# Kernel tuning notes

Measured on AMD Instinct MI355X. Metric: run time of the kernel, lower is better.

Reference implementation:

```python
import jax, jax.numpy as jnp
import numpy as np

B, S, D = 2, 2048, 4096
H, HD = 32, 128  # heads, head_dim
ROPE_BASE = 10000.0


def setup_inputs() -> dict:
    key = jax.random.key(0)
    k1, k2, k3 = jax.random.split(key, 3)
    positions = jnp.broadcast_to(jnp.arange(S, dtype=jnp.int64), (B, S))
    hidden_states = jax.random.normal(k1, (B, S, D), dtype=jnp.float32)
    W_qkv = jax.random.normal(k2, (D, 3 * D), dtype=jnp.float32) * (D ** -0.5)
    W_o = jax.random.normal(k3, (D, D), dtype=jnp.float32) * (D ** -0.5)
    return {"positions": positions, "hidden_states": hidden_states, "W_qkv": W_qkv, "W_o": W_o}


def _apply_rope(x, positions):
    # x: [B,S,H,HD]; neox-style rotate-half RoPE
    half = HD // 2
    inv_freq = 1.0 / (ROPE_BASE ** (jnp.arange(0, half, dtype=jnp.float32) / half))
    ang = positions.astype(jnp.float32)[..., None] * inv_freq  # [B,S,half]
    cos = jnp.cos(ang)[:, :, None, :]  # [B,S,1,half]
    sin = jnp.sin(ang)[:, :, None, :]
    x1, x2 = x[..., :half], x[..., half:]
    return jnp.concatenate([x1 * cos - x2 * sin, x2 * cos + x1 * sin], axis=-1)


def reference(positions, hidden_states, W_qkv, W_o):
    qkv = jnp.einsum('bsd,de->bse', hidden_states, W_qkv)
    q, k, v = jnp.split(qkv, 3, axis=-1)
    q = q.reshape(B, S, H, HD)
    k = k.reshape(B, S, H, HD)
    v = v.reshape(B, S, H, HD)
    q = _apply_rope(q, positions)
    k = _apply_rope(k, positions)
    scale = HD ** -0.5
    scores = jnp.einsum('bqhd,bkhd->bhqk', q, k) * scale
    causal = jnp.tril(jnp.ones((S, S), dtype=bool))
    scores = jnp.where(causal[None, None], scores, jnp.finfo(scores.dtype).min)
    probs = jax.nn.softmax(scores, axis=-1)
    attn = jnp.einsum('bhqk,bkhd->bqhd', probs, v).reshape(B, S, D)
    return jnp.einsum('bsd,de->bse', attn, W_o)
```

## Files before the change

kernel.cpp:

```cpp
#include <hip/hip_runtime.h>
#include <hip/hip_bf16.h>
#include <stdint.h>

typedef unsigned short u16;
typedef __attribute__((ext_vector_type(8))) short short8;
typedef __attribute__((ext_vector_type(4))) float f32x4;

__device__ __forceinline__ float bf2f(u16 u) {
  union { uint32_t i; float f; } v; v.i = ((uint32_t)u) << 16; return v.f;
}
__device__ __forceinline__ u16 f2bf(float x) {
  union { float f; uint32_t i; } v; v.f = x;
  uint32_t r = v.i + 0x7FFFu + ((v.i >> 16) & 1u);
  return (u16)(r >> 16);
}
__device__ __forceinline__ void gld16(const void* g, void* l) {
  __builtin_amdgcn_global_load_lds((const __attribute__((address_space(1))) void*)g,
                                   (__attribute__((address_space(3))) void*)l, 16, 0, 0);
}


__global__ __launch_bounds__(256) void cvt_bf16_k(const float* __restrict__ in, u16* __restrict__ out, int n) {
  int i = (blockIdx.x * 256 + threadIdx.x) * 4;
  int stride = gridDim.x * 256 * 4;
  for (; i < n; i += stride) {
    float4 v = *(const float4*)(in + i);
    ushort4 o;
    o.x = f2bf(v.x); o.y = f2bf(v.y); o.z = f2bf(v.z); o.w = f2bf(v.w);
    *(ushort4*)(out + i) = o;
  }
}

__global__ __launch_bounds__(256) void transpose_cvt_k(const float* __restrict__ W, u16* __restrict__ Wt,
                                                        int Kd, int Nd) {
  __shared__ float lds[64][68];
  int t = threadIdx.x;
  int n0 = blockIdx.x * 64, k0 = blockIdx.y * 64;
  int kr = t >> 2, cq = (t & 3) * 16;
  const float* src = W + (size_t)(k0 + kr) * Nd + n0 + cq;
  float4 a = *(const float4*)(src);
  float4 b = *(const float4*)(src + 4);
  float4 c = *(const float4*)(src + 8);
  float4 d = *(const float4*)(src + 12);
  *(float4*)&lds[kr][cq]      = a;
  *(float4*)&lds[kr][cq + 4]  = b;
  *(float4*)&lds[kr][cq + 8]  = c;
  *(float4*)&lds[kr][cq + 12] = d;
  __syncthreads();
  int rn = t >> 2, ks = (t & 3) * 16;
  u16 tmp[16];
  #pragma unroll
  for (int j = 0; j < 16; ++j) tmp[j] = f2bf(lds[ks + j][rn]);
  u16* dst = Wt + (size_t)(n0 + rn) * Kd + k0 + ks;
  *(short8*)dst       = *(short8*)tmp;
  *(short8*)(dst + 8) = *(short8*)(tmp + 8);
}

__global__ __launch_bounds__(64) void rope_table_k(const int* __restrict__ pos, float* __restrict__ tab) {
  int m = blockIdx.x, i = threadIdx.x;
  float p = (float)pos[m];
  float inv = expf(-(float)i * (9.210340371976184f / 64.0f));
  float ang = p * inv;
  float sn, cs;
  sincosf(ang, &sn, &cs);
  tab[m * 128 + i] = cs;
  tab[m * 128 + 64 + i] = sn;
}


__device__ __forceinline__ void stage_half(const u16* __restrict__ G, u16* S, int K,
                                           int tile, int half, int w, int sr, int scsw) {
  int d = tile & 1;
  int sm = half * 8 + w;
  const u16* g = G + (size_t)(sm * 16 + sr) * K + (tile << 6) + scsw;
  u16* s = S + (size_t)(d * 32 + sm * 2) * 512;
  gld16(g, s);
  gld16(g + 32, s + 512);
}

__device__ __forceinline__ short8 frag(const u16* S, int d, int sidx, int kk, int fo) {
  return *(const short8*)&S[(size_t)((d * 32 + sidx * 2 + kk) * 512) + fo];
}

template <int F32OUT>
__global__ __launch_bounds__(512) void gemm256_k(const u16* __restrict__ A, const u16* __restrict__ Bt,
                                                 void* __restrict__ Cp, int N, int K, int GX) {
  __shared__ u16 As[2 * 32 * 512];
  __shared__ u16 Bs[2 * 32 * 512];
  int lid = blockIdx.x;
  int GY = gridDim.x / GX;
  int SY = GY >> 1, SX = GX >> 2;
  int xcd = lid & 7, idx = lid >> 3;
  int ry = xcd >> 2, rx = xcd & 3;
  int bxl = idx / SY, byl = idx - bxl * SY;
  int by = ry * SY + byl, bx = rx * SX + bxl;
  int bm0 = by << 8, bn0 = bx << 8;
  int tid = threadIdx.x, w = tid >> 6, l = tid & 63;
  int wr = w >> 2, wc = w & 3;
  const u16* Ag = A + (size_t)bm0 * K;
  const u16* Bg = Bt + (size_t)bn0 * K;
  int NT = K >> 6;
  int sr = l >> 2;
  int scsw = ((l & 3) * 8) ^ ((sr & 8) ? 16 : 0);
  int fr = l & 15;
  int fo = fr * 32 + (((l >> 4) * 8) ^ ((fr & 8) ? 16 : 0));

  f32x4 acc[8][4];
  #pragma unroll
  for (int i = 0; i < 8; ++i)
    #pragma unroll
    for (int j = 0; j < 4; ++j) acc[i][j] = (f32x4){0.f, 0.f, 0.f, 0.f};

  stage_half(Ag, As, K, 0, 0, w, sr, scsw);
  stage_half(Ag, As, K, 0, 1, w, sr, scsw);
  stage_half(Bg, Bs, K, 0, 0, w, sr, scsw);
  stage_half(Bg, Bs, K, 0, 1, w, sr, scsw);
  stage_half(Ag, As, K, 1, 0, w, sr, scsw);
  asm volatile("s_waitcnt vmcnt(2)" ::: "memory");
  __builtin_amdgcn_s_barrier();
  __builtin_amdgcn_sched_barrier(0);

  for (int t = 0; t < NT; ++t) {
    int d = t & 1;
    short8 a_lo[4][2], a_hi[4][2], b_lo[2][2], b_hi[2][2];
    #pragma unroll
    for (int fm = 0; fm < 4; ++fm) {
      a_lo[fm][0] = frag(As, d, wr * 8 + fm, 0, fo);
      a_lo[fm][1] = frag(As, d, wr * 8 + fm, 1, fo);
    }
    #pragma unroll
    for (int fn = 0; fn < 2; ++fn) {
      b_lo[fn][0] = frag(Bs, d, wc * 4 + fn, 0, fo);
      b_lo[fn][1] = frag(Bs, d, wc * 4 + fn, 1, fo);
    }
    if (t + 1 < NT) stage_half(Ag, As, K, t + 1, 1, w, sr, scsw);
    __builtin_amdgcn_s_barrier();
    __builtin_amdgcn_s_setprio(1);
    #pragma unroll
    for (int fn = 0; fn < 2; ++fn) {
      b_hi[fn][0] = frag(Bs, d, wc * 4 + 2 + fn, 0, fo);
      b_hi[fn][1] = frag(Bs, d, wc * 4 + 2 + fn, 1, fo);
    }
    #pragma unroll
    for (int fm = 0; fm < 4; ++fm)
      #pragma unroll
      for (int fn = 0; fn < 2; ++fn) {
        acc[fm][fn] = __builtin_amdgcn_mfma_f32_16x16x32_bf16(a_lo[fm][0], b_lo[fn][0], acc[fm][fn], 0, 0, 0);
        acc[fm][fn] = __builtin_amdgcn_mfma_f32_16x16x32_bf16(a_lo[fm][1], b_lo[fn][1], acc[fm][fn], 0, 0, 0);
      }
    __builtin_amdgcn_s_setprio(0);
    __builtin_amdgcn_s_barrier();
    if (t + 1 < NT) stage_half(Bg, Bs, K, t + 1, 0, w, sr, scsw);
    __builtin_amdgcn_s_barrier();
    __builtin_amdgcn_s_setprio(1);
    #pragma unroll
    for (int fm = 0; fm < 4; ++fm) {
      a_hi[fm][0] = frag(As, d, wr * 8 + 4 + fm, 0, fo);
      a_hi[fm][1] = frag(As, d, wr * 8 + 4 + fm, 1, fo);
    }
    #pragma unroll
    for (int fm = 0; fm < 4; ++fm)
      #pragma unroll
      for (int fn = 0; fn < 2; ++fn) {
        acc[fm][2 + fn] = __builtin_amdgcn_mfma_f32_16x16x32_bf16(a_lo[fm][0], b_hi[fn][0], acc[fm][2 + fn], 0, 0, 0);
        acc[fm][2 + fn] = __builtin_amdgcn_mfma_f32_16x16x32_bf16(a_lo[fm][1], b_hi[fn][1], acc[fm][2 + fn], 0, 0, 0);
      }
    __builtin_amdgcn_s_setprio(0);
    __builtin_amdgcn_s_barrier();
    if (t + 1 < NT) stage_half(Bg, Bs, K, t + 1, 1, w, sr, scsw);
    __builtin_amdgcn_s_barrier();
    __builtin_amdgcn_s_setprio(1);
    #pragma unroll
    for (int fm = 0; fm < 4; ++fm)
      #pragma unroll
      for (int fn = 0; fn < 2; ++fn) {
        acc[4 + fm][2 + fn] = __builtin_amdgcn_mfma_f32_16x16x32_bf16(a_hi[fm][0], b_hi[fn][0], acc[4 + fm][2 + fn], 0, 0, 0);
        acc[4 + fm][2 + fn] = __builtin_amdgcn_mfma_f32_16x16x32_bf16(a_hi[fm][1], b_hi[fn][1], acc[4 + fm][2 + fn], 0, 0, 0);
      }
    __builtin_amdgcn_s_setprio(0);
    __builtin_amdgcn_s_barrier();
    if (t + 2 < NT) stage_half(Ag, As, K, t + 2, 0, w, sr, scsw);
    __builtin_amdgcn_s_setprio(1);
    #pragma unroll
    for (int fm = 0; fm < 4; ++fm)
      #pragma unroll
      for (int fn = 0; fn < 2; ++fn) {
        acc[4 + fm][fn] = __builtin_amdgcn_mfma_f32_16x16x32_bf16(a_hi[fm][0], b_lo[fn][0], acc[4 + fm][fn], 0, 0, 0);
        acc[4 + fm][fn] = __builtin_amdgcn_mfma_f32_16x16x32_bf16(a_hi[fm][1], b_lo[fn][1], acc[4 + fm][fn], 0, 0, 0);
      }
    __builtin_amdgcn_s_setprio(0);
    if (t + 2 < NT) asm volatile("s_waitcnt vmcnt(2)" ::: "memory");
    else            asm volatile("s_waitcnt vmcnt(0)" ::: "memory");
    __builtin_amdgcn_s_barrier();
    __builtin_amdgcn_sched_barrier(0);
  }

  int r0 = bm0 + wr * 128 + ((l >> 4) << 2);
  int c0 = bn0 + wc * 64 + (l & 15);
  #pragma unroll
  for (int fm = 0; fm < 8; ++fm)
    #pragma unroll
    for (int fn = 0; fn < 4; ++fn)
      #pragma unroll
      for (int r = 0; r < 4; ++r) {
        size_t idx2 = (size_t)(r0 + fm * 16 + r) * N + (c0 + fn * 16);
        if (F32OUT) ((float*)Cp)[idx2] = acc[fm][fn][r];
        else        ((u16*)Cp)[idx2]   = f2bf(acc[fm][fn][r]);
      }
}


__global__ __launch_bounds__(256) void rope_qk_k(const u16* __restrict__ qkv, const float* __restrict__ tab,
                                                  u16* __restrict__ Qb, u16* __restrict__ Kb) {
  int m = blockIdx.x, t = threadIdx.x;
  int b = m >> 11, s = m & 2047;
  const float* tabm = tab + m * 128;
  #pragma unroll
  for (int part = 0; part < 2; ++part) {
    const u16* src = qkv + (size_t)m * 12288 + part * 4096;
    u16* dst = part ? Kb : Qb;
    float qs = part ? 1.0f : 0.08838834764831845f;
    #pragma unroll
    for (int it = 0; it < 2; ++it) {
      int v = t + it * 256;
      int h = v >> 4;
      int d1 = (v & 15) * 4;
      const u16* sp = src + h * 128 + d1;
      ushort4 x1 = *(const ushort4*)(sp);
      ushort4 x2 = *(const ushort4*)(sp + 64);
      float4 cs = *(const float4*)(tabm + d1);
      float4 sn = *(const float4*)(tabm + 64 + d1);
      ushort4 o1, o2;
      o1.x = f2bf((bf2f(x1.x) * cs.x - bf2f(x2.x) * sn.x) * qs);
      o1.y = f2bf((bf2f(x1.y) * cs.y - bf2f(x2.y) * sn.y) * qs);
      o1.z = f2bf((bf2f(x1.z) * cs.z - bf2f(x2.z) * sn.z) * qs);
      o1.w = f2bf((bf2f(x1.w) * cs.w - bf2f(x2.w) * sn.w) * qs);
      o2.x = f2bf((bf2f(x2.x) * cs.x + bf2f(x1.x) * sn.x) * qs);
      o2.y = f2bf((bf2f(x2.y) * cs.y + bf2f(x1.y) * sn.y) * qs);
      o2.z = f2bf((bf2f(x2.z) * cs.z + bf2f(x1.z) * sn.z) * qs);
      o2.w = f2bf((bf2f(x2.w) * cs.w + bf2f(x1.w) * sn.w) * qs);
      u16* o = dst + ((size_t)(b * 32 + h) * 2048 + s) * 128 + d1;
      *(ushort4*)o        = o1;
      *(ushort4*)(o + 64) = o2;
    }
  }
}

__global__ __launch_bounds__(256) void v_transpose_k(const u16* __restrict__ qkv, u16* __restrict__ Vt) {
  __shared__ u16 lds[64][136];
  int bid = blockIdx.x;
  int bh = bid >> 5, st = bid & 31;
  int b = bh >> 5, h = bh & 31;
  int s0 = st * 64;
  int t = threadIdx.x;
  int r = t >> 2, cq = (t & 3) * 32;
  const u16* src = qkv + (size_t)(b * 2048 + s0 + r) * 12288 + 8192 + h * 128 + cq;
  *(short8*)&lds[r][cq]      = *(const short8*)(src);
  *(short8*)&lds[r][cq + 8]  = *(const short8*)(src + 8);
  *(short8*)&lds[r][cq + 16] = *(const short8*)(src + 16);
  *(short8*)&lds[r][cq + 24] = *(const short8*)(src + 24);
  __syncthreads();
  int d = t >> 1, sseg = (t & 1) * 32;
  u16 tmp[32];
  #pragma unroll
  for (int j = 0; j < 32; ++j) tmp[j] = lds[sseg + j][d];
  u16* o = Vt + (size_t)bh * (128 * 2048) + (size_t)d * 2048 + s0 + sseg;
  *(short8*)(o)      = *(short8*)(tmp);
  *(short8*)(o + 8)  = *(short8*)(tmp + 8);
  *(short8*)(o + 16) = *(short8*)(tmp + 16);
  *(short8*)(o + 24) = *(short8*)(tmp + 24);
}


__device__ __forceinline__ void stage_kv(const u16* __restrict__ Kg, const u16* __restrict__ Vg,
                                         u16* Ksb, u16* Vsb, int j0, int w, int l) {
  #pragma unroll
  for (int c = 0; c < 2; ++c) {
    int rk = c * 32 + w * 4 + (l >> 4);
    int kcol = ((l & 15) * 8) ^ ((rk & 7) << 3);
    gld16(Kg + (size_t)(j0 + rk) * 128 + kcol, Ksb + (c * 32 + w * 4) * 128);
    int rv = c * 64 + w * 8 + (l >> 3);
    int vcol = ((l & 7) * 8) ^ ((rv & 7) << 3);
    gld16(Vg + (size_t)rv * 2048 + j0 + vcol, Vsb + (c * 64 + w * 8) * 64);
  }
}

__global__ __launch_bounds__(512, 2) void attn_k(const u16* __restrict__ Qb, const u16* __restrict__ Kb,
                                                  const u16* __restrict__ Vt, u16* __restrict__ attnb) {
  __shared__ u16 Ks[2][64 * 128];
  __shared__ u16 Vs[2][128 * 64];
  __shared__ u16 Ps[8][32 * 64];
  int lid = blockIdx.x + gridDim.x * blockIdx.y;
  int xcd = lid & 7, idx = lid >> 3;
  int bh = xcd * 8 + (idx >> 3);
  int qt = idx & 7;
  int b = bh >> 5, h = bh & 31;
  int q0 = qt * 256;
  int t = threadIdx.x, w = t >> 6, l = t & 63;
  int g = l >> 4, fr = l & 15;
  const u16* Qg = Qb + (size_t)bh * (2048 * 128);
  const u16* Kg = Kb + (size_t)bh * (2048 * 128);
  const u16* Vg = Vt + (size_t)bh * (128 * 2048);

  short8 aq[2][4];
  #pragma unroll
  for (int fm = 0; fm < 2; ++fm)
    #pragma unroll
    for (int kk = 0; kk < 4; ++kk)
      aq[fm][kk] = *(const short8*)&Qg[(size_t)(q0 + w * 32 + fm * 16 + fr) * 128 + kk * 32 + g * 8];

  stage_kv(Kg, Vg, Ks[0], Vs[0], 0, w, l);
  __syncthreads();

  f32x4 zero = {0.f, 0.f, 0.f, 0.f};
  f32x4 o[2][8];
  #pragma unroll
  for (int fm = 0; fm < 2; ++fm)
    #pragma unroll
    for (int fd = 0; fd < 8; ++fd) o[fm][fd] = zero;
  float m_run[2][4], l_run[2][4];
  #pragma unroll
  for (int fm = 0; fm < 2; ++fm)
    #pragma unroll
    for (int r = 0; r < 4; ++r) { m_run[fm][r] = -1e30f; l_run[fm][r] = 0.f; }

  int NJ = 4 * qt + 4;
  for (int j = 0; j < NJ; ++j) {
    int j0 = j * 64;
    int cur = j & 1;
    if (j + 1 < NJ) stage_kv(Kg, Vg, Ks[cur ^ 1], Vs[cur ^ 1], j0 + 64, w, l);
    if (j0 < q0 + w * 32 + 32) {
      f32x4 sc[2][4];
      #pragma unroll
      for (int fm = 0; fm < 2; ++fm)
        #pragma unroll
        for (int fn = 0; fn < 4; ++fn) sc[fm][fn] = zero;
      __builtin_amdgcn_s_setprio(1);
      #pragma unroll
      for (int kk = 0; kk < 4; ++kk) {
        #pragma unroll
        for (int fn = 0; fn < 4; ++fn) {
          short8 bk = *(const short8*)&Ks[cur][(fn * 16 + fr) * 128 + ((kk * 32 + g * 8) ^ ((fr & 7) << 3))];
          #pragma unroll
          for (int fm = 0; fm < 2; ++fm)
            sc[fm][fn] = __builtin_amdgcn_mfma_f32_16x16x32_bf16(aq[fm][kk], bk, sc[fm][fn], 0, 0, 0);
        }
      }
      __builtin_amdgcn_s_setprio(0);
      int qb_ = q0 + w * 32 + (g << 2);
      int kb_ = j0 + fr;
      #pragma unroll
      for (int fm = 0; fm < 2; ++fm)
        #pragma unroll
        for (int fn = 0; fn < 4; ++fn)
          #pragma unroll
          for (int r = 0; r < 4; ++r)
            if (kb_ + fn * 16 > qb_ + fm * 16 + r) sc[fm][fn][r] = -1e30f;
      float mx[2][4];
      #pragma unroll
      for (int fm = 0; fm < 2; ++fm)
        #pragma unroll
        for (int r = 0; r < 4; ++r) {
          float v = fmaxf(fmaxf(sc[fm][0][r], sc[fm][1][r]), fmaxf(sc[fm][2][r], sc[fm][3][r]));
          v = fmaxf(v, __shfl_xor(v, 1));
          v = fmaxf(v, __shfl_xor(v, 2));
          v = fmaxf(v, __shfl_xor(v, 4));
          v = fmaxf(v, __shfl_xor(v, 8));
          mx[fm][r] = v;
        }
      float scale[2][4];
      #pragma unroll
      for (int fm = 0; fm < 2; ++fm)
        #pragma unroll
        for (int r = 0; r < 4; ++r) {
          float mn = fmaxf(m_run[fm][r], mx[fm][r]);
          scale[fm][r] = __expf(m_run[fm][r] - mn);
          m_run[fm][r] = mn;
        }
      float rs[2][4];
      #pragma unroll
      for (int fm = 0; fm < 2; ++fm)
        #pragma unroll
        for (int r = 0; r < 4; ++r) {
          float acc = 0.f;
          #pragma unroll
          for (int fn = 0; fn < 4; ++fn) {
            float p = __expf(sc[fm][fn][r] - m_run[fm][r]);
            sc[fm][fn][r] = p;
            acc += p;
          }
          acc += __shfl_xor(acc, 1);
          acc += __shfl_xor(acc, 2);
          acc += __shfl_xor(acc, 4);
          acc += __shfl_xor(acc, 8);
          rs[fm][r] = acc;
        }
      #pragma unroll
      for (int fm = 0; fm < 2; ++fm)
        #pragma unroll
        for (int r = 0; r < 4; ++r) l_run[fm][r] = l_run[fm][r] * scale[fm][r] + rs[fm][r];
      #pragma unroll
      for (int fm = 0; fm < 2; ++fm)
        #pragma unroll
        for (int fd = 0; fd < 8; ++fd)
          #pragma unroll
          for (int r = 0; r < 4; ++r) o[fm][fd][r] *= scale[fm][r];
      #pragma unroll
      for (int fm = 0; fm < 2; ++fm)
        #pragma unroll
        for (int fn = 0; fn < 4; ++fn)
          #pragma unroll
          for (int r = 0; r < 4; ++r) {
            int prow = fm * 16 + (g << 2) + r;
            Ps[w][prow * 64 + ((fn * 16 + fr) ^ ((prow & 7) << 3))] = f2bf(sc[fm][fn][r]);
          }
      __builtin_amdgcn_s_setprio(1);
      #pragma unroll
      for (int kk = 0; kk < 2; ++kk) {
        short8 pa[2];
        #pragma unroll
        for (int fm = 0; fm < 2; ++fm)
          pa[fm] = *(const short8*)&Ps[w][(fm * 16 + fr) * 64 + ((kk * 32 + g * 8) ^ ((fr & 7) << 3))];
        #pragma unroll
        for (int fd = 0; fd < 8; ++fd) {
          short8 bv = *(const short8*)&Vs[cur][(fd * 16 + fr) * 64 + ((kk * 32 + g * 8) ^ ((fr & 7) << 3))];
          #pragma unroll
          for (int fm = 0; fm < 2; ++fm)
            o[fm][fd] = __builtin_amdgcn_mfma_f32_16x16x32_bf16(pa[fm], bv, o[fm][fd], 0, 0, 0);
        }
      }
      __builtin_amdgcn_s_setprio(0);
    }
    __syncthreads();
  }

  #pragma unroll
  for (int fm = 0; fm < 2; ++fm)
    #pragma unroll
    for (int r = 0; r < 4; ++r) {
      float inv = 1.0f / l_run[fm][r];
      int srow = q0 + w * 32 + fm * 16 + (g << 2) + r;
      u16* dst = attnb + (size_t)(b * 2048 + srow) * 4096 + h * 128 + fr;
      #pragma unroll
      for (int fd = 0; fd < 8; ++fd)
        dst[fd * 16] = f2bf(o[fm][fd][r] * inv);
    }
}


extern "C" void kernel_launch(void* const* d_in, const int* in_sizes, int n_in,
                              void* d_out, int out_size, void* d_ws, size_t ws_size,
                              hipStream_t stream) {
  const int*   positions = (const int*)d_in[0];
  const float* hidden    = (const float*)d_in[1];
  const float* W_qkv     = (const float*)d_in[2];
  const float* W_o       = (const float*)d_in[3];
  float* out = (float*)d_out;
  char* ws = (char*)d_ws;

  u16* R0 = (u16*)ws;
  u16* R1 = (u16*)(ws + 100663296);
  u16* R2 = (u16*)(ws + 201326592);
  float* tab = (float*)(ws + 234881024);

  u16* hidden_bf = R2;
  u16* Wqkv_t = R0;
  u16* qkv = R1;
  u16* Qb = R2;
  u16* Kb = R0;
  u16* Vt = R0 + 16777216;
  u16* attnb = R0 + 33554432;
  u16* Wo_t = R1;

  cvt_bf16_k<<<4096, 256, 0, stream>>>(hidden, hidden_bf, 16777216);
  transpose_cvt_k<<<dim3(192, 64), 256, 0, stream>>>(W_qkv, Wqkv_t, 4096, 12288);
  rope_table_k<<<4096, 64, 0, stream>>>(positions, tab);

  gemm256_k<0><<<768, 512, 0, stream>>>(hidden_bf, Wqkv_t, qkv, 12288, 4096, 48);

  rope_qk_k<<<4096, 256, 0, stream>>>(qkv, tab, Qb, Kb);
  v_transpose_k<<<2048, 256, 0, stream>>>(qkv, Vt);
  transpose_cvt_k<<<dim3(64, 64), 256, 0, stream>>>(W_o, Wo_t, 4096, 4096);

  attn_k<<<dim3(8, 64), 512, 0, stream>>>(Qb, Kb, Vt, attnb);

  gemm256_k<1><<<256, 512, 0, stream>>>(attnb, Wo_t, out, 4096, 4096, 16);
}
```

Baseline: 894.9 us.

## Fuse RoPE, Q scaling and V transpose into QKV GEMM epilogue

```diff
diff --git a/kernel.cpp b/kernel.cpp
--- a/kernel.cpp
+++ b/kernel.cpp
@@ -57,14 +57,15 @@
 }
 
 __global__ __launch_bounds__(64) void rope_table_k(const int* __restrict__ pos, float* __restrict__ tab) {
-  int m = blockIdx.x, i = threadIdx.x;
+  int m = blockIdx.x * 64 + threadIdx.x;
   float p = (float)pos[m];
-  float inv = expf(-(float)i * (9.210340371976184f / 64.0f));
-  float ang = p * inv;
-  float sn, cs;
-  sincosf(ang, &sn, &cs);
-  tab[m * 128 + i] = cs;
-  tab[m * 128 + 64 + i] = sn;
+  for (int i = 0; i < 64; ++i) {
+    float inv = expf(-(float)i * (9.210340371976184f / 64.0f));
+    float sn, cs;
+    sincosf(p * inv, &sn, &cs);
+    tab[i * 4096 + m] = cs;
+    tab[(64 + i) * 4096 + m] = sn;
+  }
 }
 
 
@@ -82,9 +83,12 @@
   return *(const short8*)&S[(size_t)((d * 32 + sidx * 2 + kk) * 512) + fo];
 }
 
-template <int F32OUT>
+template <int MODE>
 __global__ __launch_bounds__(512) void gemm256_k(const u16* __restrict__ A, const u16* __restrict__ Bt,
-                                                 void* __restrict__ Cp, int N, int K, int GX) {
+                                                 void* __restrict__ Cp, int N, int K, int GX,
+                                                 const float* __restrict__ tab,
+                                                 u16* __restrict__ Qb, u16* __restrict__ Kb,
+                                                 u16* __restrict__ Vt) {
   __shared__ u16 As[2 * 32 * 512];
   __shared__ u16 Bs[2 * 32 * 512];
   int lid = blockIdx.x;
@@ -103,7 +107,8 @@
   int sr = l >> 2;
   int scsw = ((l & 3) * 8) ^ ((sr & 8) ? 16 : 0);
   int fr = l & 15;
-  int fo = fr * 32 + (((l >> 4) * 8) ^ ((fr & 8) ? 16 : 0));
+  int g = l >> 4;
+  int fo = fr * 32 + ((g * 8) ^ ((fr & 8) ? 16 : 0));
 
   f32x4 acc[8][4];
   #pragma unroll
@@ -137,36 +142,36 @@
     __builtin_amdgcn_s_barrier();
     __builtin_amdgcn_s_setprio(1);
     #pragma unroll
+    for (int fm = 0; fm < 4; ++fm)
+      #pragma unroll
+      for (int fn = 0; fn < 2; ++fn) {
+        acc[fm][fn] = __builtin_amdgcn_mfma_f32_16x16x32_bf16(a_lo[fm][0], b_lo[fn][0], acc[fm][fn], 0, 0, 0);
+        acc[fm][fn] = __builtin_amdgcn_mfma_f32_16x16x32_bf16(a_lo[fm][1], b_lo[fn][1], acc[fm][fn], 0, 0, 0);
+      }
+    __builtin_amdgcn_s_setprio(0);
+    __builtin_amdgcn_s_barrier();
+    #pragma unroll
     for (int fn = 0; fn < 2; ++fn) {
       b_hi[fn][0] = frag(Bs, d, wc * 4 + 2 + fn, 0, fo);
       b_hi[fn][1] = frag(Bs, d, wc * 4 + 2 + fn, 1, fo);
     }
+    if (t + 1 < NT) stage_half(Bg, Bs, K, t + 1, 0, w, sr, scsw);
+    __builtin_amdgcn_s_barrier();
+    __builtin_amdgcn_s_setprio(1);
     #pragma unroll
     for (int fm = 0; fm < 4; ++fm)
       #pragma unroll
       for (int fn = 0; fn < 2; ++fn) {
-        acc[fm][fn] = __builtin_amdgcn_mfma_f32_16x16x32_bf16(a_lo[fm][0], b_lo[fn][0], acc[fm][fn], 0, 0, 0);
-        acc[fm][fn] = __builtin_amdgcn_mfma_f32_16x16x32_bf16(a_lo[fm][1], b_lo[fn][1], acc[fm][fn], 0, 0, 0);
+        acc[fm][2 + fn] = __builtin_amdgcn_mfma_f32_16x16x32_bf16(a_lo[fm][0], b_hi[fn][0], acc[fm][2 + fn], 0, 0, 0);
+        acc[fm][2 + fn] = __builtin_amdgcn_mfma_f32_16x16x32_bf16(a_lo[fm][1], b_hi[fn][1], acc[fm][2 + fn], 0, 0, 0);
       }
     __builtin_amdgcn_s_setprio(0);
     __builtin_amdgcn_s_barrier();
-    if (t + 1 < NT) stage_half(Bg, Bs, K, t + 1, 0, w, sr, scsw);
-    __builtin_amdgcn_s_barrier();
-    __builtin_amdgcn_s_setprio(1);
     #pragma unroll
     for (int fm = 0; fm < 4; ++fm) {
       a_hi[fm][0] = frag(As, d, wr * 8 + 4 + fm, 0, fo);
       a_hi[fm][1] = frag(As, d, wr * 8 + 4 + fm, 1, fo);
     }
-    #pragma unroll
-    for (int fm = 0; fm < 4; ++fm)
-      #pragma unroll
-      for (int fn = 0; fn < 2; ++fn) {
-        acc[fm][2 + fn] = __builtin_amdgcn_mfma_f32_16x16x32_bf16(a_lo[fm][0], b_hi[fn][0], acc[fm][2 + fn], 0, 0, 0);
-        acc[fm][2 + fn] = __builtin_amdgcn_mfma_f32_16x16x32_bf16(a_lo[fm][1], b_hi[fn][1], acc[fm][2 + fn], 0, 0, 0);
-      }
-    __builtin_amdgcn_s_setprio(0);
-    __builtin_amdgcn_s_barrier();
     if (t + 1 < NT) stage_half(Bg, Bs, K, t + 1, 1, w, sr, scsw);
     __builtin_amdgcn_s_barrier();
     __builtin_amdgcn_s_setprio(1);
@@ -195,80 +200,75 @@
     __builtin_amdgcn_sched_barrier(0);
   }
 
-  int r0 = bm0 + wr * 128 + ((l >> 4) << 2);
-  int c0 = bn0 + wc * 64 + (l & 15);
-  #pragma unroll
-  for (int fm = 0; fm < 8; ++fm)
-    #pragma unroll
-    for (int fn = 0; fn < 4; ++fn)
-      #pragma unroll
-      for (int r = 0; r < 4; ++r) {
-        size_t idx2 = (size_t)(r0 + fm * 16 + r) * N + (c0 + fn * 16);
-        if (F32OUT) ((float*)Cp)[idx2] = acc[fm][fn][r];
-        else        ((u16*)Cp)[idx2]   = f2bf(acc[fm][fn][r]);
-      }
-}
-
-
-__global__ __launch_bounds__(256) void rope_qk_k(const u16* __restrict__ qkv, const float* __restrict__ tab,
-                                                  u16* __restrict__ Qb, u16* __restrict__ Kb) {
-  int m = blockIdx.x, t = threadIdx.x;
-  int b = m >> 11, s = m & 2047;
-  const float* tabm = tab + m * 128;
-  #pragma unroll
-  for (int part = 0; part < 2; ++part) {
-    const u16* src = qkv + (size_t)m * 12288 + part * 4096;
-    u16* dst = part ? Kb : Qb;
-    float qs = part ? 1.0f : 0.08838834764831845f;
-    #pragma unroll
-    for (int it = 0; it < 2; ++it) {
-      int v = t + it * 256;
-      int h = v >> 4;
-      int d1 = (v & 15) * 4;
-      const u16* sp = src + h * 128 + d1;
-      ushort4 x1 = *(const ushort4*)(sp);
-      ushort4 x2 = *(const ushort4*)(sp + 64);
-      float4 cs = *(const float4*)(tabm + d1);
-      float4 sn = *(const float4*)(tabm + 64 + d1);
-      ushort4 o1, o2;
-      o1.x = f2bf((bf2f(x1.x) * cs.x - bf2f(x2.x) * sn.x) * qs);
-      o1.y = f2bf((bf2f(x1.y) * cs.y - bf2f(x2.y) * sn.y) * qs);
-      o1.z = f2bf((bf2f(x1.z) * cs.z - bf2f(x2.z) * sn.z) * qs);
-      o1.w = f2bf((bf2f(x1.w) * cs.w - bf2f(x2.w) * sn.w) * qs);
-      o2.x = f2bf((bf2f(x2.x) * cs.x + bf2f(x1.x) * sn.x) * qs);
-      o2.y = f2bf((bf2f(x2.y) * cs.y + bf2f(x1.y) * sn.y) * qs);
-      o2.z = f2bf((bf2f(x2.z) * cs.z + bf2f(x1.z) * sn.z) * qs);
-      o2.w = f2bf((bf2f(x2.w) * cs.w + bf2f(x1.w) * sn.w) * qs);
-      u16* o = dst + ((size_t)(b * 32 + h) * 2048 + s) * 128 + d1;
-      *(ushort4*)o        = o1;
-      *(ushort4*)(o + 64) = o2;
-    }
-  }
-}
-
-__global__ __launch_bounds__(256) void v_transpose_k(const u16* __restrict__ qkv, u16* __restrict__ Vt) {
-  __shared__ u16 lds[64][136];
-  int bid = blockIdx.x;
-  int bh = bid >> 5, st = bid & 31;
-  int b = bh >> 5, h = bh & 31;
-  int s0 = st * 64;
-  int t = threadIdx.x;
-  int r = t >> 2, cq = (t & 3) * 32;
-  const u16* src = qkv + (size_t)(b * 2048 + s0 + r) * 12288 + 8192 + h * 128 + cq;
-  *(short8*)&lds[r][cq]      = *(const short8*)(src);
-  *(short8*)&lds[r][cq + 8]  = *(const short8*)(src + 8);
-  *(short8*)&lds[r][cq + 16] = *(const short8*)(src + 16);
-  *(short8*)&lds[r][cq + 24] = *(const short8*)(src + 24);
-  __syncthreads();
-  int d = t >> 1, sseg = (t & 1) * 32;
-  u16 tmp[32];
-  #pragma unroll
-  for (int j = 0; j < 32; ++j) tmp[j] = lds[sseg + j][d];
-  u16* o = Vt + (size_t)bh * (128 * 2048) + (size_t)d * 2048 + s0 + sseg;
-  *(short8*)(o)      = *(short8*)(tmp);
-  *(short8*)(o + 8)  = *(short8*)(tmp + 8);
-  *(short8*)(o + 16) = *(short8*)(tmp + 16);
-  *(short8*)(o + 24) = *(short8*)(tmp + 24);
+  if (MODE == 1) {
+    int r0 = bm0 + wr * 128 + (g << 2);
+    int c0 = bn0 + wc * 64 + fr;
+    #pragma unroll
+    for (int fm = 0; fm < 8; ++fm)
+      #pragma unroll
+      for (int fn = 0; fn < 4; ++fn)
+        #pragma unroll
+        for (int r = 0; r < 4; ++r) {
+          size_t idx2 = (size_t)(r0 + fm * 16 + r) * N + (c0 + fn * 16);
+          ((float*)Cp)[idx2] = acc[fm][fn][r];
+        }
+  } else {
+    int seg = bn0 >> 12;
+    int cb_base = bn0 & 4095;
+    int b_ = bm0 >> 11;
+    int s_base = bm0 & 2047;
+    int g4 = g << 2;
+    if (seg < 2) {
+      float qs = (seg == 0) ? 0.08838834764831845f : 1.0f;
+      u16* dstb = (seg == 0) ? Qb : Kb;
+      float* xch = (float*)As;
+      #pragma unroll 1
+      for (int fm = 0; fm < 8; ++fm) {
+        #pragma unroll
+        for (int fn = 0; fn < 4; ++fn)
+          #pragma unroll
+          for (int r = 0; r < 4; ++r)
+            xch[(w * 16 + g4 + r) * 65 + fn * 16 + fr] = acc[fm][fn][r];
+        __syncthreads();
+        #pragma unroll
+        for (int fn = 0; fn < 4; ++fn) {
+          int cb = wc * 64 + fn * 16 + fr;
+          int d = cb & 127;
+          int hh = (cb_base + cb) >> 7;
+          int i = d & 63;
+          int srow = s_base + wr * 128 + fm * 16 + g4;
+          int mbase = b_ * 2048 + srow;
+          float4 cs4 = *(const float4*)&tab[(size_t)i * 4096 + mbase];
+          float4 sn4 = *(const float4*)&tab[(size_t)(64 + i) * 4096 + mbase];
+          u16* dst = dstb + ((size_t)(b_ * 32 + hh) * 2048 + srow) * 128 + d;
+          float csa[4] = {cs4.x, cs4.y, cs4.z, cs4.w};
+          float sna[4] = {sn4.x, sn4.y, sn4.z, sn4.w};
+          #pragma unroll
+          for (int r = 0; r < 4; ++r) {
+            float own = acc[fm][fn][r];
+            float part = xch[((w ^ 1) * 16 + g4 + r) * 65 + fn * 16 + fr];
+            float val = (d < 64) ? (own * csa[r] - part * sna[r]) : (own * csa[r] + part * sna[r]);
+            dst[(size_t)r * 128] = f2bf(val * qs);
+          }
+        }
+        __syncthreads();
+      }
+    } else {
+      #pragma unroll
+      for (int fm = 0; fm < 8; ++fm)
+        #pragma unroll
+        for (int fn = 0; fn < 4; ++fn) {
+          int cb = wc * 64 + fn * 16 + fr;
+          int d = cb & 127;
+          int hh = (cb_base + cb) >> 7;
+          int srow = s_base + wr * 128 + fm * 16 + g4;
+          ushort4 t4;
+          t4.x = f2bf(acc[fm][fn][0]); t4.y = f2bf(acc[fm][fn][1]);
+          t4.z = f2bf(acc[fm][fn][2]); t4.w = f2bf(acc[fm][fn][3]);
+          *(ushort4*)(Vt + (size_t)(b_ * 32 + hh) * (128 * 2048) + (size_t)d * 2048 + srow) = t4;
+        }
+    }
+  }
 }
 
 
@@ -292,8 +292,8 @@
   __shared__ u16 Ps[8][32 * 64];
   int lid = blockIdx.x + gridDim.x * blockIdx.y;
   int xcd = lid & 7, idx = lid >> 3;
-  int bh = xcd * 8 + (idx >> 3);
-  int qt = idx & 7;
+  int bh = xcd * 8 + (idx & 7);
+  int qt = 7 - (idx >> 3);
   int b = bh >> 5, h = bh & 31;
   int q0 = qt * 256;
   int t = threadIdx.x, w = t >> 6, l = t & 63;
@@ -458,31 +458,26 @@
   float* out = (float*)d_out;
   char* ws = (char*)d_ws;
 
-  u16* R0 = (u16*)ws;
-  u16* R1 = (u16*)(ws + 100663296);
-  u16* R2 = (u16*)(ws + 201326592);
-  float* tab = (float*)(ws + 234881024);
-
-  u16* hidden_bf = R2;
-  u16* Wqkv_t = R0;
-  u16* qkv = R1;
-  u16* Qb = R2;
-  u16* Kb = R0;
-  u16* Vt = R0 + 16777216;
-  u16* attnb = R0 + 33554432;
-  u16* Wo_t = R1;
+  u16* Wqkv_t    = (u16*)(ws + 0);
+  u16* Wo_t      = (u16*)(ws + 0);
+  u16* Qb        = (u16*)(ws + 100663296);
+  u16* Kb        = (u16*)(ws + 134217728);
+  u16* Vt        = (u16*)(ws + 167772160);
+  u16* hidden_bf = (u16*)(ws + 201326592);
+  u16* attnb     = (u16*)(ws + 201326592);
+  float* tab     = (float*)(ws + 234881024);
 
   cvt_bf16_k<<<4096, 256, 0, stream>>>(hidden, hidden_bf, 16777216);
   transpose_cvt_k<<<dim3(192, 64), 256, 0, stream>>>(W_qkv, Wqkv_t, 4096, 12288);
-  rope_table_k<<<4096, 64, 0, stream>>>(positions, tab);
-
-  gemm256_k<0><<<768, 512, 0, stream>>>(hidden_bf, Wqkv_t, qkv, 12288, 4096, 48);
-
-  rope_qk_k<<<4096, 256, 0, stream>>>(qkv, tab, Qb, Kb);
-  v_transpose_k<<<2048, 256, 0, stream>>>(qkv, Vt);
+  rope_table_k<<<64, 64, 0, stream>>>(positions, tab);
+
+  gemm256_k<2><<<768, 512, 0, stream>>>(hidden_bf, Wqkv_t, nullptr, 12288, 4096, 48,
+                                        tab, Qb, Kb, Vt);
+
   transpose_cvt_k<<<dim3(64, 64), 256, 0, stream>>>(W_o, Wo_t, 4096, 4096);
 
   attn_k<<<dim3(8, 64), 512, 0, stream>>>(Qb, Kb, Vt, attnb);
 
-  gemm256_k<1><<<256, 512, 0, stream>>>(attnb, Wo_t, out, 4096, 4096, 16);
-}
+  gemm256_k<1><<<256, 512, 0, stream>>>(attnb, Wo_t, out, 4096, 4096, 16,
+                                        nullptr, nullptr, nullptr, nullptr);
+}
```

Measured after the change: 927.6 us. 3.7% more time.
